# Kernel tuning notes

Measured on AMD Instinct MI355X. Metric: run time of the kernel, lower is better.

## Reference

```python
import jax, jax.numpy as jnp
import numpy as np
import math

DIM = 1024
HEADS = 16
B, N = 2, 2048

POLY = jnp.array([-0.037, 0.481, -2.3, 4.917, -1.791], dtype=jnp.float32)


def adaptive_temperature_softmax(logits):
    # logits: [b, h, n, n]
    original_probs = jax.nn.softmax(logits, axis=-1)
    entropy = jnp.sum(-original_probs * jnp.log(original_probs + 1e-9), axis=-1, keepdims=True)
    e2 = entropy * entropy
    poly_result = POLY[0] * e2 * e2 + POLY[1] * e2 * entropy + POLY[2] * e2 + POLY[3] * entropy + POLY[4]
    beta = jnp.where(entropy > 0.5, jnp.maximum(poly_result, 1.0), 1.0)
    return jax.nn.softmax(logits * beta, axis=-1)


def setup_inputs() -> dict:
    key = jax.random.key(0)
    ks = jax.random.split(key, 5)
    s = 1.0 / math.sqrt(DIM)
    return {
        "x": jax.random.normal(ks[0], (B, N, DIM), dtype=jnp.float32),
        "Wq": jax.random.normal(ks[1], (DIM, DIM), dtype=jnp.float32) * s,
        "Wk": jax.random.normal(ks[2], (DIM, DIM), dtype=jnp.float32) * s,
        "Wv": jax.random.normal(ks[3], (DIM, DIM), dtype=jnp.float32) * s,
        "Wo": jax.random.normal(ks[4], (DIM, DIM), dtype=jnp.float32) * s,
        "bo": jnp.zeros((DIM,), dtype=jnp.float32),
    }


def reference(x, Wq, Wk, Wv, Wo, bo):
    b, n, d = x.shape
    h = HEADS
    hd = d // h
    # torch nn.Linear: y = x @ W.T (+ bias)
    def proj(W):
        t = x @ W.T  # [b, n, d]
        return t.reshape(b, n, h, hd).transpose(0, 2, 1, 3)  # [b, h, n, hd]
    q, k, v = proj(Wq), proj(Wk), proj(Wv)
    sim = jnp.einsum('bhid,bhjd->bhij', q, k) / math.sqrt(hd)
    neg = -jnp.finfo(sim.dtype).max
    causal = jnp.triu(jnp.ones((n, n), dtype=bool), k=1)  # True above diagonal
    sim = jnp.where(causal, neg, sim)
    attn = adaptive_temperature_softmax(sim)
    out = jnp.einsum('bhij,bhjd->bhid', attn, v)
    out = out.transpose(0, 2, 1, 3).reshape(b, n, d)
    return out @ Wo.T + bo
```

## Files before the change

### kernel.cpp

```cpp
#include <hip/hip_runtime.h>
#include <math.h>

#define B_   2
#define N_   2048
#define D_   1024
#define H_   16
#define HD_  64
#define BH_  32
#define M_   4096

typedef __bf16 bf16x8 __attribute__((ext_vector_type(8)));
typedef float  f32x4  __attribute__((ext_vector_type(4)));

__device__ inline unsigned short f2b(float f) {
    unsigned u = __float_as_uint(f);
    u += 0x7FFFu + ((u >> 16) & 1u);
    return (unsigned short)(u >> 16);
}
__device__ inline unsigned short f2b_fast(float f) {
    return (unsigned short)((__float_as_uint(f) + 0x8000u) >> 16);
}

__global__ __launch_bounds__(256)
void cvt_all(const float* __restrict__ x,  const float* __restrict__ wq,
             const float* __restrict__ wk, const float* __restrict__ wv,
             const float* __restrict__ wo, ushort* __restrict__ dst)
{
    int i = blockIdx.x * 256 + threadIdx.x;
    if (i >= 2097152) return;
    int fi = i * 4;
    const float* s; int off;
    if (fi < 4194304) { s = x; off = fi; }
    else {
        int r = fi - 4194304;
        int wsel = r >> 20;
        off = r & 1048575;
        s = (wsel == 0) ? wq : (wsel == 1) ? wk : (wsel == 2) ? wv : wo;
    }
    float4 f = *(const float4*)(s + off);
    ushort4 o;
    o.x = f2b(f.x); o.y = f2b(f.y); o.z = f2b(f.z); o.w = f2b(f.w);
    *(ushort4*)(dst + fi) = o;
}

__global__ __launch_bounds__(256)
void gemm_qkv(const ushort* __restrict__ A,
              const ushort* __restrict__ W0, const ushort* __restrict__ W1,
              const ushort* __restrict__ W2,
              ushort* __restrict__ O0, ushort* __restrict__ O1,
              ushort* __restrict__ O2)
{
    const int z = blockIdx.z;
    const ushort* W = (z == 0) ? W0 : (z == 1) ? W1 : W2;

    __shared__ alignas(16) ushort As[128][40];
    __shared__ alignas(16) ushort Bs[128][40];

    const int t = threadIdx.x;
    const int lane = t & 63, w = t >> 6;
    const int quad = lane >> 4, l15 = lane & 15;
    const int wm = (w >> 1) * 64, wn = (w & 1) * 64;
    const int tileM = blockIdx.x * 128, tileN = blockIdx.y * 128;

    const int r0 = t >> 2, r1 = 64 + (t >> 2);
    const int cg = (t & 3) * 8;
    const ushort* GA0 = A + (size_t)(tileM + r0) * D_ + cg;
    const ushort* GA1 = A + (size_t)(tileM + r1) * D_ + cg;
    const ushort* GB0 = W + (size_t)(tileN + r0) * D_ + cg;
    const ushort* GB1 = W + (size_t)(tileN + r1) * D_ + cg;

    f32x4 acc[4][4];
#pragma unroll
    for (int mt = 0; mt < 4; ++mt)
#pragma unroll
        for (int nt = 0; nt < 4; ++nt) acc[mt][nt] = (f32x4){0.f, 0.f, 0.f, 0.f};

    uint4 pa0 = *(const uint4*)GA0, pa1 = *(const uint4*)GA1;
    uint4 pb0 = *(const uint4*)GB0, pb1 = *(const uint4*)GB1;

    for (int k0 = 0; k0 < D_; k0 += 32) {
        __syncthreads();
        *(uint4*)&As[r0][cg] = pa0;
        *(uint4*)&As[r1][cg] = pa1;
        *(uint4*)&Bs[r0][cg] = pb0;
        *(uint4*)&Bs[r1][cg] = pb1;
        __syncthreads();
        if (k0 + 32 < D_) {
            pa0 = *(const uint4*)(GA0 + k0 + 32);
            pa1 = *(const uint4*)(GA1 + k0 + 32);
            pb0 = *(const uint4*)(GB0 + k0 + 32);
            pb1 = *(const uint4*)(GB1 + k0 + 32);
        }

        bf16x8 af[4], bf[4];
#pragma unroll
        for (int mt = 0; mt < 4; ++mt) af[mt] = *(const bf16x8*)&As[wm + mt * 16 + l15][quad * 8];
#pragma unroll
        for (int nt = 0; nt < 4; ++nt) bf[nt] = *(const bf16x8*)&Bs[wn + nt * 16 + l15][quad * 8];
#pragma unroll
        for (int mt = 0; mt < 4; ++mt)
#pragma unroll
            for (int nt = 0; nt < 4; ++nt)
                acc[mt][nt] = __builtin_amdgcn_mfma_f32_16x16x32_bf16(af[mt], bf[nt], acc[mt][nt], 0, 0, 0);
    }

    ushort* O = (z == 0) ? O0 : (z == 1) ? O1 : O2;
    const float scl = (z == 0) ? 0.18033688f : 1.0f;
#pragma unroll
    for (int mt = 0; mt < 4; ++mt)
#pragma unroll
        for (int nt = 0; nt < 4; ++nt) {
            if (z == 2) {
                int rg0 = tileM + wm + mt * 16 + quad * 4;
                int cgc = tileN + wn + nt * 16 + l15;
                int b = rg0 >> 11, n0 = rg0 & (N_ - 1);
                int h = cgc >> 6, dd = cgc & 63;
                ushort4 o4;
                o4.x = f2b(acc[mt][nt][0]); o4.y = f2b(acc[mt][nt][1]);
                o4.z = f2b(acc[mt][nt][2]); o4.w = f2b(acc[mt][nt][3]);
                *(ushort4*)&O[((size_t)((b * H_ + h) * HD_ + dd)) * N_ + n0] = o4;
            } else {
#pragma unroll
                for (int r = 0; r < 4; ++r) {
                    int rg = tileM + wm + mt * 16 + quad * 4 + r;
                    int cgc = tileN + wn + nt * 16 + l15;
                    int b = rg >> 11, n = rg & (N_ - 1);
                    int h = cgc >> 6, dd = cgc & 63;
                    O[(((size_t)(b * H_ + h)) * N_ + n) * HD_ + dd] = f2b(acc[mt][nt][r] * scl);
                }
            }
        }
}

__global__ __launch_bounds__(256)
void gemm_fin(const ushort* __restrict__ A, const ushort* __restrict__ W,
              const float* __restrict__ bias, float* __restrict__ Of)
{
    __shared__ alignas(16) ushort As[128][40];
    __shared__ alignas(16) ushort Bs[64][40];

    const int t = threadIdx.x;
    const int lane = t & 63, w = t >> 6;
    const int quad = lane >> 4, l15 = lane & 15;
    const int wm = (w >> 1) * 64, wn = (w & 1) * 32;
    const int tileM = blockIdx.x * 128, tileN = blockIdx.y * 64;

    const int r0 = t >> 2, r1 = 64 + (t >> 2);
    const int cg = (t & 3) * 8;
    const ushort* GA0 = A + (size_t)(tileM + r0) * D_ + cg;
    const ushort* GA1 = A + (size_t)(tileM + r1) * D_ + cg;
    const ushort* GB0 = W + (size_t)(tileN + r0) * D_ + cg;

    f32x4 acc[4][2];
#pragma unroll
    for (int mt = 0; mt < 4; ++mt)
#pragma unroll
        for (int nt = 0; nt < 2; ++nt) acc[mt][nt] = (f32x4){0.f, 0.f, 0.f, 0.f};

    uint4 pa0 = *(const uint4*)GA0, pa1 = *(const uint4*)GA1;
    uint4 pb0 = *(const uint4*)GB0;

    for (int k0 = 0; k0 < D_; k0 += 32) {
        __syncthreads();
        *(uint4*)&As[r0][cg] = pa0;
        *(uint4*)&As[r1][cg] = pa1;
        *(uint4*)&Bs[r0 & 63][cg] = pb0;
        __syncthreads();
        if (k0 + 32 < D_) {
            pa0 = *(const uint4*)(GA0 + k0 + 32);
            pa1 = *(const uint4*)(GA1 + k0 + 32);
            pb0 = *(const uint4*)(GB0 + k0 + 32);
        }

        bf16x8 af[4], bf[2];
#pragma unroll
        for (int mt = 0; mt < 4; ++mt) af[mt] = *(const bf16x8*)&As[wm + mt * 16 + l15][quad * 8];
#pragma unroll
        for (int nt = 0; nt < 2; ++nt) bf[nt] = *(const bf16x8*)&Bs[wn + nt * 16 + l15][quad * 8];
#pragma unroll
        for (int mt = 0; mt < 4; ++mt)
#pragma unroll
            for (int nt = 0; nt < 2; ++nt)
                acc[mt][nt] = __builtin_amdgcn_mfma_f32_16x16x32_bf16(af[mt], bf[nt], acc[mt][nt], 0, 0, 0);
    }

#pragma unroll
    for (int mt = 0; mt < 4; ++mt)
#pragma unroll
        for (int nt = 0; nt < 2; ++nt)
#pragma unroll
            for (int r = 0; r < 4; ++r) {
                int rg = tileM + wm + mt * 16 + quad * 4 + r;
                int cgc = tileN + wn + nt * 16 + l15;
                Of[(size_t)rg * D_ + cgc] = acc[mt][nt][r] + bias[cgc];
            }
}

__global__ __launch_bounds__(256)
void attn_mfma(const ushort* __restrict__ Q, const ushort* __restrict__ K,
               const ushort* __restrict__ VT, ushort* __restrict__ AO)
{
    const int bid = blockIdx.x;
    const int p  = bid >> 5;
    const int bh = bid & 31;
    const size_t kvbase = (size_t)bh * N_ * HD_;

    __shared__ alignas(16) ushort Ks[64][72];
    __shared__ alignas(16) ushort Vt[64][72];
    __shared__ alignas(16) ushort Ps[4][4][296];

    const int t = threadIdx.x;
    const int lane = t & 63, w = t >> 6;
    const int quad = lane >> 4, l15 = lane & 15;
    const float SH2 = 11.5416913f;
    const float LN2 = 0.69314718f;

    const int skey = t >> 3;
    const int skc  = (t & 7) * 8;
    const ushort* KS0 = K  + kvbase + (size_t)skey * HD_ + skc;
    const ushort* KS1 = KS0 + 32 * HD_;
    const ushort* VS0 = VT + kvbase + (size_t)skey * N_ + skc;
    const ushort* VS1 = VS0 + 32 * N_;

    const int qrow = w * 16 + quad * 4;
    const int b = bh >> 4, h = bh & 15;

    for (int item = 0; item < 2; ++item) {
        const int qt = item ? p : (31 - p);

        bf16x8 aq0, aq1;
        {
            const size_t qr = kvbase + (size_t)(qt * 64 + w * 16 + l15) * HD_;
            aq0 = *(const bf16x8*)&Q[qr + quad * 8];
            aq1 = *(const bf16x8*)&Q[qr + 32 + quad * 8];
        }

        float ez[4] = {0.f, 0.f, 0.f, 0.f};
        float sz[4] = {0.f, 0.f, 0.f, 0.f};

        uint4 pk0 = *(const uint4*)KS0;
        uint4 pk1 = *(const uint4*)KS1;
        for (int kb = 0; kb <= qt; ++kb) {
            __syncthreads();
            *(uint4*)&Ks[skey][skc]      = pk0;
            *(uint4*)&Ks[32 + skey][skc] = pk1;
            __syncthreads();
            if (kb < qt) {
                pk0 = *(const uint4*)(KS0 + (size_t)(kb + 1) * (64 * HD_));
                pk1 = *(const uint4*)(KS1 + (size_t)(kb + 1) * (64 * HD_));
            }
            if (kb < qt) {
#pragma unroll
                for (int nt = 0; nt < 4; ++nt) {
                    f32x4 sv = (f32x4){0.f, 0.f, 0.f, 0.f};
                    sv = __builtin_amdgcn_mfma_f32_16x16x32_bf16(aq0, *(const bf16x8*)&Ks[nt * 16 + l15][quad * 8], sv, 0, 0, 0);
                    sv = __builtin_amdgcn_mfma_f32_16x16x32_bf16(aq1, *(const bf16x8*)&Ks[nt * 16 + l15][32 + quad * 8], sv, 0, 0, 0);
#pragma unroll
                    for (int r = 0; r < 4; ++r) {
                        float sh = sv[r] - SH2;
                        float e = __builtin_amdgcn_exp2f(sh);
                        ez[r] += e;
                        sz[r] = fmaf(e, sh, sz[r]);
                    }
                }
            } else {
#pragma unroll
                for (int nt = 0; nt < 4; ++nt) {
                    f32x4 sv = (f32x4){0.f, 0.f, 0.f, 0.f};
                    sv = __builtin_amdgcn_mfma_f32_16x16x32_bf16(aq0, *(const bf16x8*)&Ks[nt * 16 + l15][quad * 8], sv, 0, 0, 0);
                    sv = __builtin_amdgcn_mfma_f32_16x16x32_bf16(aq1, *(const bf16x8*)&Ks[nt * 16 + l15][32 + quad * 8], sv, 0, 0, 0);
                    const int kcol = nt * 16 + l15;
#pragma unroll
                    for (int r = 0; r < 4; ++r) {
                        float sh = sv[r] - SH2;
                        float e = (kcol <= qrow + r) ? __builtin_amdgcn_exp2f(sh) : 0.f;
                        ez[r] += e;
                        sz[r] = fmaf(e, sh, sz[r]);
                    }
                }
            }
        }
#pragma unroll
        for (int r = 0; r < 4; ++r) {
#pragma unroll
            for (int off = 1; off < 16; off <<= 1) {
                ez[r] += __shfl_xor(ez[r], off);
                sz[r] += __shfl_xor(sz[r], off);
            }
        }

        float nbs[4], bl[4];
#pragma unroll
        for (int r = 0; r < 4; ++r) {
            float Z = ez[r];
            float Hh = LN2 * (__builtin_amdgcn_logf(Z) - sz[r] / Z);
            float bb = 1.f;
            if (Hh > 0.5f) {
                float e2 = Hh * Hh;
                float pp = -0.037f * e2 * e2 + 0.481f * e2 * Hh - 2.3f * e2 + 4.917f * Hh - 1.791f;
                bb = fmaxf(pp, 1.f);
            }
            bl[r] = bb;
            nbs[r] = -bb * SH2;
        }

        f32x4 ov[4];
#pragma unroll
        for (int nt = 0; nt < 4; ++nt) ov[nt] = (f32x4){0.f, 0.f, 0.f, 0.f};
        float zp[4] = {0.f, 0.f, 0.f, 0.f};

        pk0 = *(const uint4*)KS0;
        pk1 = *(const uint4*)KS1;
        uint4 pv0 = *(const uint4*)VS0;
        uint4 pv1 = *(const uint4*)VS1;
        for (int kb = 0; kb <= qt; ++kb) {
            __syncthreads();
            *(uint4*)&Ks[skey][skc]      = pk0;
            *(uint4*)&Ks[32 + skey][skc] = pk1;
            *(uint4*)&Vt[skey][skc]      = pv0;
            *(uint4*)&Vt[32 + skey][skc] = pv1;
            __syncthreads();
            if (kb < qt) {
                pk0 = *(const uint4*)(KS0 + (size_t)(kb + 1) * (64 * HD_));
                pk1 = *(const uint4*)(KS1 + (size_t)(kb + 1) * (64 * HD_));
                pv0 = *(const uint4*)(VS0 + (kb + 1) * 64);
                pv1 = *(const uint4*)(VS1 + (kb + 1) * 64);
            }
            const bool diag = (kb == qt);

            float wv[4][4];
#pragma unroll
            for (int nt = 0; nt < 4; ++nt) {
                f32x4 sv = (f32x4){0.f, 0.f, 0.f, 0.f};
                sv = __builtin_amdgcn_mfma_f32_16x16x32_bf16(aq0, *(const bf16x8*)&Ks[nt * 16 + l15][quad * 8], sv, 0, 0, 0);
                sv = __builtin_amdgcn_mfma_f32_16x16x32_bf16(aq1, *(const bf16x8*)&Ks[nt * 16 + l15][32 + quad * 8], sv, 0, 0, 0);
                const int kcol = nt * 16 + l15;
#pragma unroll
                for (int r = 0; r < 4; ++r) {
                    float e = __builtin_amdgcn_exp2f(fmaf(bl[r], sv[r], nbs[r]));
                    wv[nt][r] = (!diag || (kcol <= qrow + r)) ? e : 0.f;
                }
            }
#pragma unroll
            for (int nt = 0; nt < 4; ++nt)
#pragma unroll
                for (int r = 0; r < 4; ++r)
                    Ps[w][quad][r * 72 + nt * 16 + l15] = f2b_fast(wv[nt][r]);
#pragma unroll
            for (int r = 0; r < 4; ++r)
                zp[r] += (wv[0][r] + wv[1][r]) + (wv[2][r] + wv[3][r]);

            bf16x8 pa0 = *(const bf16x8*)&Ps[w][l15 >> 2][(l15 & 3) * 72 + quad * 8];
            bf16x8 pa1 = *(const bf16x8*)&Ps[w][l15 >> 2][(l15 & 3) * 72 + 32 + quad * 8];
#pragma unroll
            for (int nt = 0; nt < 4; ++nt) {
                ov[nt] = __builtin_amdgcn_mfma_f32_16x16x32_bf16(pa0, *(const bf16x8*)&Vt[nt * 16 + l15][quad * 8], ov[nt], 0, 0, 0);
                ov[nt] = __builtin_amdgcn_mfma_f32_16x16x32_bf16(pa1, *(const bf16x8*)&Vt[nt * 16 + l15][32 + quad * 8], ov[nt], 0, 0, 0);
            }
        }
#pragma unroll
        for (int r = 0; r < 4; ++r)
#pragma unroll
            for (int off = 1; off < 16; off <<= 1) zp[r] += __shfl_xor(zp[r], off);

#pragma unroll
        for (int r = 0; r < 4; ++r) {
            int qg = qt * 64 + w * 16 + quad * 4 + r;
            float inv = 1.f / zp[r];
            size_t rowoff = ((size_t)(b * N_ + qg)) * D_ + h * HD_;
#pragma unroll
            for (int nt = 0; nt < 4; ++nt)
                AO[rowoff + nt * 16 + l15] = f2b(ov[nt][r] * inv);
        }
    }
}

extern "C" void kernel_launch(void* const* d_in, const int* in_sizes, int n_in,
                              void* d_out, int out_size, void* d_ws, size_t ws_size,
                              hipStream_t stream)
{
    const float* x  = (const float*)d_in[0];
    const float* Wq = (const float*)d_in[1];
    const float* Wk = (const float*)d_in[2];
    const float* Wv = (const float*)d_in[3];
    const float* Wo = (const float*)d_in[4];
    const float* bo = (const float*)d_in[5];
    float* out = (float*)d_out;

    ushort* ws  = (ushort*)d_ws;
    ushort* xb  = ws;
    ushort* wqb = ws + 4194304;
    ushort* wkb = ws + 5242880;
    ushort* wvb = ws + 6291456;
    ushort* wob = ws + 7340032;
    ushort* Qb  = ws + 8388608;
    ushort* Kb  = ws + 12582912;
    ushort* Vtb = ws + 16777216;
    ushort* aob = ws + 20971520;

    cvt_all<<<8192, 256, 0, stream>>>(x, Wq, Wk, Wv, Wo, xb);

    gemm_qkv<<<dim3(32, 8, 3), 256, 0, stream>>>(
        xb, wqb, wkb, wvb, Qb, Kb, Vtb);

    attn_mfma<<<dim3(512), 256, 0, stream>>>(Qb, Kb, Vtb, aob);

    gemm_fin<<<dim3(32, 16), 256, 0, stream>>>(aob, wob, bo, out);
}
```

Measured before the change: 207.1 us.

## Fuse fp32-to-bf16 conversion into GEMMs and split attention into one q-tile per block

Removes the separate conversion kernel, so the QKV and output GEMMs now load fp32 inputs and weights directly and pack them to bf16 before writing to shared memory. The attention kernel drops the paired-item scheme and launches 1024 blocks, each handling a single query tile. Its entropy pass now streams 128-key chunks through a merged K/V shared buffer. This saves a launch and a full fp32-to-bf16 round trip through memory, but doubles global load bytes in the GEMMs and gives up the causal load balancing of pairing.

```diff
diff --git a/kernel.cpp b/kernel.cpp
--- a/kernel.cpp
+++ b/kernel.cpp
@@ -20,38 +20,24 @@
 __device__ inline unsigned short f2b_fast(float f) {
     return (unsigned short)((__float_as_uint(f) + 0x8000u) >> 16);
 }
+__device__ inline uint4 pk8(float4 a, float4 b) {
+    uint4 u;
+    u.x = (uint)f2b(a.x) | ((uint)f2b(a.y) << 16);
+    u.y = (uint)f2b(a.z) | ((uint)f2b(a.w) << 16);
+    u.z = (uint)f2b(b.x) | ((uint)f2b(b.y) << 16);
+    u.w = (uint)f2b(b.z) | ((uint)f2b(b.w) << 16);
+    return u;
+}
 
 __global__ __launch_bounds__(256)
-void cvt_all(const float* __restrict__ x,  const float* __restrict__ wq,
-             const float* __restrict__ wk, const float* __restrict__ wv,
-             const float* __restrict__ wo, ushort* __restrict__ dst)
-{
-    int i = blockIdx.x * 256 + threadIdx.x;
-    if (i >= 2097152) return;
-    int fi = i * 4;
-    const float* s; int off;
-    if (fi < 4194304) { s = x; off = fi; }
-    else {
-        int r = fi - 4194304;
-        int wsel = r >> 20;
-        off = r & 1048575;
-        s = (wsel == 0) ? wq : (wsel == 1) ? wk : (wsel == 2) ? wv : wo;
-    }
-    float4 f = *(const float4*)(s + off);
-    ushort4 o;
-    o.x = f2b(f.x); o.y = f2b(f.y); o.z = f2b(f.z); o.w = f2b(f.w);
-    *(ushort4*)(dst + fi) = o;
-}
-
-__global__ __launch_bounds__(256)
-void gemm_qkv(const ushort* __restrict__ A,
-              const ushort* __restrict__ W0, const ushort* __restrict__ W1,
-              const ushort* __restrict__ W2,
+void gemm_qkv(const float* __restrict__ X,
+              const float* __restrict__ W0, const float* __restrict__ W1,
+              const float* __restrict__ W2,
               ushort* __restrict__ O0, ushort* __restrict__ O1,
               ushort* __restrict__ O2)
 {
     const int z = blockIdx.z;
-    const ushort* W = (z == 0) ? W0 : (z == 1) ? W1 : W2;
+    const float* W = (z == 0) ? W0 : (z == 1) ? W1 : W2;
 
     __shared__ alignas(16) ushort As[128][40];
     __shared__ alignas(16) ushort Bs[128][40];
@@ -64,10 +50,10 @@
 
     const int r0 = t >> 2, r1 = 64 + (t >> 2);
     const int cg = (t & 3) * 8;
-    const ushort* GA0 = A + (size_t)(tileM + r0) * D_ + cg;
-    const ushort* GA1 = A + (size_t)(tileM + r1) * D_ + cg;
-    const ushort* GB0 = W + (size_t)(tileN + r0) * D_ + cg;
-    const ushort* GB1 = W + (size_t)(tileN + r1) * D_ + cg;
+    const float* GA0 = X + (size_t)(tileM + r0) * D_ + cg;
+    const float* GA1 = X + (size_t)(tileM + r1) * D_ + cg;
+    const float* GB0 = W + (size_t)(tileN + r0) * D_ + cg;
+    const float* GB1 = W + (size_t)(tileN + r1) * D_ + cg;
 
     f32x4 acc[4][4];
 #pragma unroll
@@ -75,21 +61,23 @@
 #pragma unroll
         for (int nt = 0; nt < 4; ++nt) acc[mt][nt] = (f32x4){0.f, 0.f, 0.f, 0.f};
 
-    uint4 pa0 = *(const uint4*)GA0, pa1 = *(const uint4*)GA1;
-    uint4 pb0 = *(const uint4*)GB0, pb1 = *(const uint4*)GB1;
+    float4 a00 = *(const float4*)GA0, a01 = *(const float4*)(GA0 + 4);
+    float4 a10 = *(const float4*)GA1, a11 = *(const float4*)(GA1 + 4);
+    float4 b00 = *(const float4*)GB0, b01 = *(const float4*)(GB0 + 4);
+    float4 b10 = *(const float4*)GB1, b11 = *(const float4*)(GB1 + 4);
 
     for (int k0 = 0; k0 < D_; k0 += 32) {
         __syncthreads();
-        *(uint4*)&As[r0][cg] = pa0;
-        *(uint4*)&As[r1][cg] = pa1;
-        *(uint4*)&Bs[r0][cg] = pb0;
-        *(uint4*)&Bs[r1][cg] = pb1;
+        *(uint4*)&As[r0][cg] = pk8(a00, a01);
+        *(uint4*)&As[r1][cg] = pk8(a10, a11);
+        *(uint4*)&Bs[r0][cg] = pk8(b00, b01);
+        *(uint4*)&Bs[r1][cg] = pk8(b10, b11);
         __syncthreads();
         if (k0 + 32 < D_) {
-            pa0 = *(const uint4*)(GA0 + k0 + 32);
-            pa1 = *(const uint4*)(GA1 + k0 + 32);
-            pb0 = *(const uint4*)(GB0 + k0 + 32);
-            pb1 = *(const uint4*)(GB1 + k0 + 32);
+            a00 = *(const float4*)(GA0 + k0 + 32); a01 = *(const float4*)(GA0 + k0 + 36);
+            a10 = *(const float4*)(GA1 + k0 + 32); a11 = *(const float4*)(GA1 + k0 + 36);
+            b00 = *(const float4*)(GB0 + k0 + 32); b01 = *(const float4*)(GB0 + k0 + 36);
+            b10 = *(const float4*)(GB1 + k0 + 32); b11 = *(const float4*)(GB1 + k0 + 36);
         }
 
         bf16x8 af[4], bf[4];
@@ -133,7 +121,7 @@
 }
 
 __global__ __launch_bounds__(256)
-void gemm_fin(const ushort* __restrict__ A, const ushort* __restrict__ W,
+void gemm_fin(const ushort* __restrict__ A, const float* __restrict__ W,
               const float* __restrict__ bias, float* __restrict__ Of)
 {
     __shared__ alignas(16) ushort As[128][40];
@@ -149,7 +137,7 @@
     const int cg = (t & 3) * 8;
     const ushort* GA0 = A + (size_t)(tileM + r0) * D_ + cg;
     const ushort* GA1 = A + (size_t)(tileM + r1) * D_ + cg;
-    const ushort* GB0 = W + (size_t)(tileN + r0) * D_ + cg;
+    const float*  GB0 = W + (size_t)(tileN + r0) * D_ + cg;
 
     f32x4 acc[4][2];
 #pragma unroll
@@ -157,19 +145,20 @@
 #pragma unroll
         for (int nt = 0; nt < 2; ++nt) acc[mt][nt] = (f32x4){0.f, 0.f, 0.f, 0.f};
 
-    uint4 pa0 = *(const uint4*)GA0, pa1 = *(const uint4*)GA1;
-    uint4 pb0 = *(const uint4*)GB0;
+    uint4  pa0 = *(const uint4*)GA0, pa1 = *(const uint4*)GA1;
+    float4 b00 = *(const float4*)GB0, b01 = *(const float4*)(GB0 + 4);
 
     for (int k0 = 0; k0 < D_; k0 += 32) {
         __syncthreads();
         *(uint4*)&As[r0][cg] = pa0;
         *(uint4*)&As[r1][cg] = pa1;
-        *(uint4*)&Bs[r0 & 63][cg] = pb0;
+        *(uint4*)&Bs[r0 & 63][cg] = pk8(b00, b01);
         __syncthreads();
         if (k0 + 32 < D_) {
             pa0 = *(const uint4*)(GA0 + k0 + 32);
             pa1 = *(const uint4*)(GA1 + k0 + 32);
-            pb0 = *(const uint4*)(GB0 + k0 + 32);
+            b00 = *(const float4*)(GB0 + k0 + 32);
+            b01 = *(const float4*)(GB0 + k0 + 36);
         }
 
         bf16x8 af[4], bf[2];
@@ -201,12 +190,11 @@
                const ushort* __restrict__ VT, ushort* __restrict__ AO)
 {
     const int bid = blockIdx.x;
-    const int p  = bid >> 5;
+    const int qt = 31 - (bid >> 5);
     const int bh = bid & 31;
     const size_t kvbase = (size_t)bh * N_ * HD_;
 
-    __shared__ alignas(16) ushort Ks[64][72];
-    __shared__ alignas(16) ushort Vt[64][72];
+    __shared__ alignas(16) ushort KV[128][72];
     __shared__ alignas(16) ushort Ps[4][4][296];
 
     const int t = threadIdx.x;
@@ -217,161 +205,169 @@
 
     const int skey = t >> 3;
     const int skc  = (t & 7) * 8;
-    const ushort* KS0 = K  + kvbase + (size_t)skey * HD_ + skc;
-    const ushort* KS1 = KS0 + 32 * HD_;
+    const ushort* KS = K  + kvbase + (size_t)skey * HD_ + skc;
     const ushort* VS0 = VT + kvbase + (size_t)skey * N_ + skc;
     const ushort* VS1 = VS0 + 32 * N_;
 
     const int qrow = w * 16 + quad * 4;
     const int b = bh >> 4, h = bh & 15;
 
-    for (int item = 0; item < 2; ++item) {
-        const int qt = item ? p : (31 - p);
-
-        bf16x8 aq0, aq1;
-        {
-            const size_t qr = kvbase + (size_t)(qt * 64 + w * 16 + l15) * HD_;
-            aq0 = *(const bf16x8*)&Q[qr + quad * 8];
-            aq1 = *(const bf16x8*)&Q[qr + 32 + quad * 8];
-        }
-
-        float ez[4] = {0.f, 0.f, 0.f, 0.f};
-        float sz[4] = {0.f, 0.f, 0.f, 0.f};
-
-        uint4 pk0 = *(const uint4*)KS0;
-        uint4 pk1 = *(const uint4*)KS1;
-        for (int kb = 0; kb <= qt; ++kb) {
-            __syncthreads();
-            *(uint4*)&Ks[skey][skc]      = pk0;
-            *(uint4*)&Ks[32 + skey][skc] = pk1;
-            __syncthreads();
-            if (kb < qt) {
-                pk0 = *(const uint4*)(KS0 + (size_t)(kb + 1) * (64 * HD_));
-                pk1 = *(const uint4*)(KS1 + (size_t)(kb + 1) * (64 * HD_));
-            }
-            if (kb < qt) {
-#pragma unroll
-                for (int nt = 0; nt < 4; ++nt) {
-                    f32x4 sv = (f32x4){0.f, 0.f, 0.f, 0.f};
-                    sv = __builtin_amdgcn_mfma_f32_16x16x32_bf16(aq0, *(const bf16x8*)&Ks[nt * 16 + l15][quad * 8], sv, 0, 0, 0);
-                    sv = __builtin_amdgcn_mfma_f32_16x16x32_bf16(aq1, *(const bf16x8*)&Ks[nt * 16 + l15][32 + quad * 8], sv, 0, 0, 0);
-#pragma unroll
-                    for (int r = 0; r < 4; ++r) {
-                        float sh = sv[r] - SH2;
-                        float e = __builtin_amdgcn_exp2f(sh);
-                        ez[r] += e;
-                        sz[r] = fmaf(e, sh, sz[r]);
-                    }
+    bf16x8 aq0, aq1;
+    {
+        const size_t qr = kvbase + (size_t)(qt * 64 + w * 16 + l15) * HD_;
+        aq0 = *(const bf16x8*)&Q[qr + quad * 8];
+        aq1 = *(const bf16x8*)&Q[qr + 32 + quad * 8];
+    }
+
+    float ez[4] = {0.f, 0.f, 0.f, 0.f};
+    float sz[4] = {0.f, 0.f, 0.f, 0.f};
+
+    const int nfull = qt >> 1;
+    const int lastTiles = (((qt + 1) * 64) - nfull * 128) >> 4;
+
+    uint4 q0 = *(const uint4*)KS;
+    uint4 q1 = *(const uint4*)(KS + 32 * HD_);
+    uint4 q2 = *(const uint4*)(KS + 64 * HD_);
+    uint4 q3 = *(const uint4*)(KS + 96 * HD_);
+
+    for (int c = 0; c <= nfull; ++c) {
+        __syncthreads();
+        *(uint4*)&KV[skey][skc]      = q0;
+        *(uint4*)&KV[32 + skey][skc] = q1;
+        *(uint4*)&KV[64 + skey][skc] = q2;
+        *(uint4*)&KV[96 + skey][skc] = q3;
+        __syncthreads();
+        if (c < nfull) {
+            const ushort* nb = KS + (size_t)(c + 1) * (128 * HD_);
+            q0 = *(const uint4*)nb;
+            q1 = *(const uint4*)(nb + 32 * HD_);
+            q2 = *(const uint4*)(nb + 64 * HD_);
+            q3 = *(const uint4*)(nb + 96 * HD_);
+        }
+        if (c < nfull) {
+#pragma unroll
+            for (int nt = 0; nt < 8; ++nt) {
+                f32x4 sv = (f32x4){0.f, 0.f, 0.f, 0.f};
+                sv = __builtin_amdgcn_mfma_f32_16x16x32_bf16(aq0, *(const bf16x8*)&KV[nt * 16 + l15][quad * 8], sv, 0, 0, 0);
+                sv = __builtin_amdgcn_mfma_f32_16x16x32_bf16(aq1, *(const bf16x8*)&KV[nt * 16 + l15][32 + quad * 8], sv, 0, 0, 0);
+#pragma unroll
+                for (int r = 0; r < 4; ++r) {
+                    float sh = sv[r] - SH2;
+                    float e = __builtin_amdgcn_exp2f(sh);
+                    ez[r] += e;
+                    sz[r] = fmaf(e, sh, sz[r]);
                 }
-            } else {
-#pragma unroll
-                for (int nt = 0; nt < 4; ++nt) {
-                    f32x4 sv = (f32x4){0.f, 0.f, 0.f, 0.f};
-                    sv = __builtin_amdgcn_mfma_f32_16x16x32_bf16(aq0, *(const bf16x8*)&Ks[nt * 16 + l15][quad * 8], sv, 0, 0, 0);
-                    sv = __builtin_amdgcn_mfma_f32_16x16x32_bf16(aq1, *(const bf16x8*)&Ks[nt * 16 + l15][32 + quad * 8], sv, 0, 0, 0);
-                    const int kcol = nt * 16 + l15;
-#pragma unroll
-                    for (int r = 0; r < 4; ++r) {
-                        float sh = sv[r] - SH2;
-                        float e = (kcol <= qrow + r) ? __builtin_amdgcn_exp2f(sh) : 0.f;
-                        ez[r] += e;
-                        sz[r] = fmaf(e, sh, sz[r]);
-                    }
+            }
+        } else {
+            const int kbase = c * 128;
+            const int qglob = qt * 64 + qrow;
+            for (int nt = 0; nt < lastTiles; ++nt) {
+                f32x4 sv = (f32x4){0.f, 0.f, 0.f, 0.f};
+                sv = __builtin_amdgcn_mfma_f32_16x16x32_bf16(aq0, *(const bf16x8*)&KV[nt * 16 + l15][quad * 8], sv, 0, 0, 0);
+                sv = __builtin_amdgcn_mfma_f32_16x16x32_bf16(aq1, *(const bf16x8*)&KV[nt * 16 + l15][32 + quad * 8], sv, 0, 0, 0);
+                const int kcol = kbase + nt * 16 + l15;
+#pragma unroll
+                for (int r = 0; r < 4; ++r) {
+                    float sh = sv[r] - SH2;
+                    float e = (kcol <= qglob + r) ? __builtin_amdgcn_exp2f(sh) : 0.f;
+                    ez[r] += e;
+                    sz[r] = fmaf(e, sh, sz[r]);
                 }
             }
         }
-#pragma unroll
-        for (int r = 0; r < 4; ++r) {
-#pragma unroll
-            for (int off = 1; off < 16; off <<= 1) {
-                ez[r] += __shfl_xor(ez[r], off);
-                sz[r] += __shfl_xor(sz[r], off);
-            }
-        }
-
-        float nbs[4], bl[4];
-#pragma unroll
-        for (int r = 0; r < 4; ++r) {
-            float Z = ez[r];
-            float Hh = LN2 * (__builtin_amdgcn_logf(Z) - sz[r] / Z);
-            float bb = 1.f;
-            if (Hh > 0.5f) {
-                float e2 = Hh * Hh;
-                float pp = -0.037f * e2 * e2 + 0.481f * e2 * Hh - 2.3f * e2 + 4.917f * Hh - 1.791f;
-                bb = fmaxf(pp, 1.f);
-            }
-            bl[r] = bb;
-            nbs[r] = -bb * SH2;
-        }
-
-        f32x4 ov[4];
-#pragma unroll
-        for (int nt = 0; nt < 4; ++nt) ov[nt] = (f32x4){0.f, 0.f, 0.f, 0.f};
-        float zp[4] = {0.f, 0.f, 0.f, 0.f};
-
-        pk0 = *(const uint4*)KS0;
-        pk1 = *(const uint4*)KS1;
-        uint4 pv0 = *(const uint4*)VS0;
-        uint4 pv1 = *(const uint4*)VS1;
-        for (int kb = 0; kb <= qt; ++kb) {
-            __syncthreads();
-            *(uint4*)&Ks[skey][skc]      = pk0;
-            *(uint4*)&Ks[32 + skey][skc] = pk1;
-            *(uint4*)&Vt[skey][skc]      = pv0;
-            *(uint4*)&Vt[32 + skey][skc] = pv1;
-            __syncthreads();
-            if (kb < qt) {
-                pk0 = *(const uint4*)(KS0 + (size_t)(kb + 1) * (64 * HD_));
-                pk1 = *(const uint4*)(KS1 + (size_t)(kb + 1) * (64 * HD_));
-                pv0 = *(const uint4*)(VS0 + (kb + 1) * 64);
-                pv1 = *(const uint4*)(VS1 + (kb + 1) * 64);
-            }
-            const bool diag = (kb == qt);
-
-            float wv[4][4];
-#pragma unroll
-            for (int nt = 0; nt < 4; ++nt) {
-                f32x4 sv = (f32x4){0.f, 0.f, 0.f, 0.f};
-                sv = __builtin_amdgcn_mfma_f32_16x16x32_bf16(aq0, *(const bf16x8*)&Ks[nt * 16 + l15][quad * 8], sv, 0, 0, 0);
-                sv = __builtin_amdgcn_mfma_f32_16x16x32_bf16(aq1, *(const bf16x8*)&Ks[nt * 16 + l15][32 + quad * 8], sv, 0, 0, 0);
-                const int kcol = nt * 16 + l15;
-#pragma unroll
-                for (int r = 0; r < 4; ++r) {
-                    float e = __builtin_amdgcn_exp2f(fmaf(bl[r], sv[r], nbs[r]));
-                    wv[nt][r] = (!diag || (kcol <= qrow + r)) ? e : 0.f;
-                }
-            }
-#pragma unroll
-            for (int nt = 0; nt < 4; ++nt)
-#pragma unroll
-                for (int r = 0; r < 4; ++r)
-                    Ps[w][quad][r * 72 + nt * 16 + l15] = f2b_fast(wv[nt][r]);
+    }
+#pragma unroll
+    for (int r = 0; r < 4; ++r) {
+#pragma unroll
+        for (int off = 1; off < 16; off <<= 1) {
+            ez[r] += __shfl_xor(ez[r], off);
+            sz[r] += __shfl_xor(sz[r], off);
+        }
+    }
+
+    float nbs[4], bl[4];
+#pragma unroll
+    for (int r = 0; r < 4; ++r) {
+        float Z = ez[r];
+        float Hh = LN2 * (__builtin_amdgcn_logf(Z) - sz[r] / Z);
+        float bb = 1.f;
+        if (Hh > 0.5f) {
+            float e2 = Hh * Hh;
+            float pp = -0.037f * e2 * e2 + 0.481f * e2 * Hh - 2.3f * e2 + 4.917f * Hh - 1.791f;
+            bb = fmaxf(pp, 1.f);
+        }
+        bl[r] = bb;
+        nbs[r] = -bb * SH2;
+    }
+
+    f32x4 ov[4];
+#pragma unroll
+    for (int nt = 0; nt < 4; ++nt) ov[nt] = (f32x4){0.f, 0.f, 0.f, 0.f};
+    float zp[4] = {0.f, 0.f, 0.f, 0.f};
+
+    uint4 pk0 = *(const uint4*)KS;
+    uint4 pk1 = *(const uint4*)(KS + 32 * HD_);
+    uint4 pv0 = *(const uint4*)VS0;
+    uint4 pv1 = *(const uint4*)VS1;
+    for (int kb = 0; kb <= qt; ++kb) {
+        __syncthreads();
+        *(uint4*)&KV[skey][skc]      = pk0;
+        *(uint4*)&KV[32 + skey][skc] = pk1;
+        *(uint4*)&KV[64 + skey][skc] = pv0;
+        *(uint4*)&KV[96 + skey][skc] = pv1;
+        __syncthreads();
+        if (kb < qt) {
+            const ushort* nk = KS + (size_t)(kb + 1) * (64 * HD_);
+            pk0 = *(const uint4*)nk;
+            pk1 = *(const uint4*)(nk + 32 * HD_);
+            pv0 = *(const uint4*)(VS0 + (kb + 1) * 64);
+            pv1 = *(const uint4*)(VS1 + (kb + 1) * 64);
+        }
+        const bool diag = (kb == qt);
+
+        float wv[4][4];
+#pragma unroll
+        for (int nt = 0; nt < 4; ++nt) {
+            f32x4 sv = (f32x4){0.f, 0.f, 0.f, 0.f};
+            sv = __builtin_amdgcn_mfma_f32_16x16x32_bf16(aq0, *(const bf16x8*)&KV[nt * 16 + l15][quad * 8], sv, 0, 0, 0);
+            sv = __builtin_amdgcn_mfma_f32_16x16x32_bf16(aq1, *(const bf16x8*)&KV[nt * 16 + l15][32 + quad * 8], sv, 0, 0, 0);
+            const int kcol = nt * 16 + l15;
+#pragma unroll
+            for (int r = 0; r < 4; ++r) {
+                float e = __builtin_amdgcn_exp2f(fmaf(bl[r], sv[r], nbs[r]));
+                wv[nt][r] = (!diag || (kcol <= qrow + r)) ? e : 0.f;
+            }
+        }
+#pragma unroll
+        for (int nt = 0; nt < 4; ++nt)
 #pragma unroll
             for (int r = 0; r < 4; ++r)
-                zp[r] += (wv[0][r] + wv[1][r]) + (wv[2][r] + wv[3][r]);
-
-            bf16x8 pa0 = *(const bf16x8*)&Ps[w][l15 >> 2][(l15 & 3) * 72 + quad * 8];
-            bf16x8 pa1 = *(const bf16x8*)&Ps[w][l15 >> 2][(l15 & 3) * 72 + 32 + quad * 8];
-#pragma unroll
-            for (int nt = 0; nt < 4; ++nt) {
-                ov[nt] = __builtin_amdgcn_mfma_f32_16x16x32_bf16(pa0, *(const bf16x8*)&Vt[nt * 16 + l15][quad * 8], ov[nt], 0, 0, 0);
-                ov[nt] = __builtin_amdgcn_mfma_f32_16x16x32_bf16(pa1, *(const bf16x8*)&Vt[nt * 16 + l15][32 + quad * 8], ov[nt], 0, 0, 0);
-            }
-        }
+                Ps[w][quad][r * 72 + nt * 16 + l15] = f2b_fast(wv[nt][r]);
 #pragma unroll
         for (int r = 0; r < 4; ++r)
-#pragma unroll
-            for (int off = 1; off < 16; off <<= 1) zp[r] += __shfl_xor(zp[r], off);
-
-#pragma unroll
-        for (int r = 0; r < 4; ++r) {
-            int qg = qt * 64 + w * 16 + quad * 4 + r;
-            float inv = 1.f / zp[r];
-            size_t rowoff = ((size_t)(b * N_ + qg)) * D_ + h * HD_;
-#pragma unroll
-            for (int nt = 0; nt < 4; ++nt)
-                AO[rowoff + nt * 16 + l15] = f2b(ov[nt][r] * inv);
-        }
+            zp[r] += (wv[0][r] + wv[1][r]) + (wv[2][r] + wv[3][r]);
+
+        bf16x8 pa0 = *(const bf16x8*)&Ps[w][l15 >> 2][(l15 & 3) * 72 + quad * 8];
+        bf16x8 pa1 = *(const bf16x8*)&Ps[w][l15 >> 2][(l15 & 3) * 72 + 32 + quad * 8];
+#pragma unroll
+        for (int nt = 0; nt < 4; ++nt) {
+            ov[nt] = __builtin_amdgcn_mfma_f32_16x16x32_bf16(pa0, *(const bf16x8*)&KV[64 + nt * 16 + l15][quad * 8], ov[nt], 0, 0, 0);
+            ov[nt] = __builtin_amdgcn_mfma_f32_16x16x32_bf16(pa1, *(const bf16x8*)&KV[64 + nt * 16 + l15][32 + quad * 8], ov[nt], 0, 0, 0);
+        }
+    }
+#pragma unroll
+    for (int r = 0; r < 4; ++r)
+#pragma unroll
+        for (int off = 1; off < 16; off <<= 1) zp[r] += __shfl_xor(zp[r], off);
+
+#pragma unroll
+    for (int r = 0; r < 4; ++r) {
+        int qg = qt * 64 + w * 16 + quad * 4 + r;
+        float inv = 1.f / zp[r];
+        size_t rowoff = ((size_t)(b * N_ + qg)) * D_ + h * HD_;
+#pragma unroll
+        for (int nt = 0; nt < 4; ++nt)
+            AO[rowoff + nt * 16 + l15] = f2b(ov[nt][r] * inv);
     }
 }
 
@@ -388,22 +384,15 @@
     float* out = (float*)d_out;
 
     ushort* ws  = (ushort*)d_ws;
-    ushort* xb  = ws;
-    ushort* wqb = ws + 4194304;
-    ushort* wkb = ws + 5242880;
-    ushort* wvb = ws + 6291456;
-    ushort* wob = ws + 7340032;
-    ushort* Qb  = ws + 8388608;
-    ushort* Kb  = ws + 12582912;
-    ushort* Vtb = ws + 16777216;
-    ushort* aob = ws + 20971520;
-
-    cvt_all<<<8192, 256, 0, stream>>>(x, Wq, Wk, Wv, Wo, xb);
+    ushort* Qb  = ws;
+    ushort* Kb  = ws + 4194304;
+    ushort* Vtb = ws + 8388608;
+    ushort* aob = ws + 12582912;
 
     gemm_qkv<<<dim3(32, 8, 3), 256, 0, stream>>>(
-        xb, wqb, wkb, wvb, Qb, Kb, Vtb);
-
-    attn_mfma<<<dim3(512), 256, 0, stream>>>(Qb, Kb, Vtb, aob);
-
-    gemm_fin<<<dim3(32, 16), 256, 0, stream>>>(aob, wob, bo, out);
-}
+        x, Wq, Wk, Wv, Qb, Kb, Vtb);
+
+    attn_mfma<<<dim3(1024), 256, 0, stream>>>(Qb, Kb, Vtb, aob);
+
+    gemm_fin<<<dim3(32, 16), 256, 0, stream>>>(aob, Wo, bo, out);
+}
```

New measurement: 215.4 us. 1.04x slower.

## Split attention into one q-tile per block and fuse Wo conversion into final GEMM

Applied to the files above, without the earlier changes.

The attention kernel now launches one block per (query tile, head) in descending tile-size order, replacing the paired-tile blocks that balanced the causal workload by hand. The output-projection GEMM reads fp32 Wo directly and converts it to bf16 while staging into shared memory, so the conversion kernel no longer processes Wo. This increases the block count and occupancy options for attention, but depends on hardware scheduling for balance. The GEMM now reads twice the weight bytes and repeats the conversion in every M-tile block.

```diff
diff --git a/kernel.cpp b/kernel.cpp
--- a/kernel.cpp
+++ b/kernel.cpp
@@ -20,14 +20,22 @@
 __device__ inline unsigned short f2b_fast(float f) {
     return (unsigned short)((__float_as_uint(f) + 0x8000u) >> 16);
 }
+__device__ inline uint4 pk8(float4 a, float4 b) {
+    uint4 u;
+    u.x = (uint)f2b(a.x) | ((uint)f2b(a.y) << 16);
+    u.y = (uint)f2b(a.z) | ((uint)f2b(a.w) << 16);
+    u.z = (uint)f2b(b.x) | ((uint)f2b(b.y) << 16);
+    u.w = (uint)f2b(b.z) | ((uint)f2b(b.w) << 16);
+    return u;
+}
 
 __global__ __launch_bounds__(256)
-void cvt_all(const float* __restrict__ x,  const float* __restrict__ wq,
-             const float* __restrict__ wk, const float* __restrict__ wv,
-             const float* __restrict__ wo, ushort* __restrict__ dst)
+void cvt_xw(const float* __restrict__ x,  const float* __restrict__ wq,
+            const float* __restrict__ wk, const float* __restrict__ wv,
+            ushort* __restrict__ dst)
 {
     int i = blockIdx.x * 256 + threadIdx.x;
-    if (i >= 2097152) return;
+    if (i >= 1835008) return;
     int fi = i * 4;
     const float* s; int off;
     if (fi < 4194304) { s = x; off = fi; }
@@ -35,7 +43,7 @@
         int r = fi - 4194304;
         int wsel = r >> 20;
         off = r & 1048575;
-        s = (wsel == 0) ? wq : (wsel == 1) ? wk : (wsel == 2) ? wv : wo;
+        s = (wsel == 0) ? wq : (wsel == 1) ? wk : wv;
     }
     float4 f = *(const float4*)(s + off);
     ushort4 o;
@@ -133,7 +141,7 @@
 }
 
 __global__ __launch_bounds__(256)
-void gemm_fin(const ushort* __restrict__ A, const ushort* __restrict__ W,
+void gemm_fin(const ushort* __restrict__ A, const float* __restrict__ W,
               const float* __restrict__ bias, float* __restrict__ Of)
 {
     __shared__ alignas(16) ushort As[128][40];
@@ -149,7 +157,7 @@
     const int cg = (t & 3) * 8;
     const ushort* GA0 = A + (size_t)(tileM + r0) * D_ + cg;
     const ushort* GA1 = A + (size_t)(tileM + r1) * D_ + cg;
-    const ushort* GB0 = W + (size_t)(tileN + r0) * D_ + cg;
+    const float*  GB0 = W + (size_t)(tileN + r0) * D_ + cg;
 
     f32x4 acc[4][2];
 #pragma unroll
@@ -157,19 +165,20 @@
 #pragma unroll
         for (int nt = 0; nt < 2; ++nt) acc[mt][nt] = (f32x4){0.f, 0.f, 0.f, 0.f};
 
-    uint4 pa0 = *(const uint4*)GA0, pa1 = *(const uint4*)GA1;
-    uint4 pb0 = *(const uint4*)GB0;
+    uint4  pa0 = *(const uint4*)GA0, pa1 = *(const uint4*)GA1;
+    float4 b00 = *(const float4*)GB0, b01 = *(const float4*)(GB0 + 4);
 
     for (int k0 = 0; k0 < D_; k0 += 32) {
         __syncthreads();
         *(uint4*)&As[r0][cg] = pa0;
         *(uint4*)&As[r1][cg] = pa1;
-        *(uint4*)&Bs[r0 & 63][cg] = pb0;
+        *(uint4*)&Bs[r0 & 63][cg] = pk8(b00, b01);
         __syncthreads();
         if (k0 + 32 < D_) {
             pa0 = *(const uint4*)(GA0 + k0 + 32);
             pa1 = *(const uint4*)(GA1 + k0 + 32);
-            pb0 = *(const uint4*)(GB0 + k0 + 32);
+            b00 = *(const float4*)(GB0 + k0 + 32);
+            b01 = *(const float4*)(GB0 + k0 + 36);
         }
 
         bf16x8 af[4], bf[2];
@@ -201,7 +210,7 @@
                const ushort* __restrict__ VT, ushort* __restrict__ AO)
 {
     const int bid = blockIdx.x;
-    const int p  = bid >> 5;
+    const int qt = 31 - (bid >> 5);
     const int bh = bid & 31;
     const size_t kvbase = (size_t)bh * N_ * HD_;
 
@@ -225,110 +234,42 @@
     const int qrow = w * 16 + quad * 4;
     const int b = bh >> 4, h = bh & 15;
 
-    for (int item = 0; item < 2; ++item) {
-        const int qt = item ? p : (31 - p);
-
-        bf16x8 aq0, aq1;
-        {
-            const size_t qr = kvbase + (size_t)(qt * 64 + w * 16 + l15) * HD_;
-            aq0 = *(const bf16x8*)&Q[qr + quad * 8];
-            aq1 = *(const bf16x8*)&Q[qr + 32 + quad * 8];
-        }
-
-        float ez[4] = {0.f, 0.f, 0.f, 0.f};
-        float sz[4] = {0.f, 0.f, 0.f, 0.f};
-
-        uint4 pk0 = *(const uint4*)KS0;
-        uint4 pk1 = *(const uint4*)KS1;
-        for (int kb = 0; kb <= qt; ++kb) {
-            __syncthreads();
-            *(uint4*)&Ks[skey][skc]      = pk0;
-            *(uint4*)&Ks[32 + skey][skc] = pk1;
-            __syncthreads();
-            if (kb < qt) {
-                pk0 = *(const uint4*)(KS0 + (size_t)(kb + 1) * (64 * HD_));
-                pk1 = *(const uint4*)(KS1 + (size_t)(kb + 1) * (64 * HD_));
-            }
-            if (kb < qt) {
-#pragma unroll
-                for (int nt = 0; nt < 4; ++nt) {
-                    f32x4 sv = (f32x4){0.f, 0.f, 0.f, 0.f};
-                    sv = __builtin_amdgcn_mfma_f32_16x16x32_bf16(aq0, *(const bf16x8*)&Ks[nt * 16 + l15][quad * 8], sv, 0, 0, 0);
-                    sv = __builtin_amdgcn_mfma_f32_16x16x32_bf16(aq1, *(const bf16x8*)&Ks[nt * 16 + l15][32 + quad * 8], sv, 0, 0, 0);
-#pragma unroll
-                    for (int r = 0; r < 4; ++r) {
-                        float sh = sv[r] - SH2;
-                        float e = __builtin_amdgcn_exp2f(sh);
-                        ez[r] += e;
-                        sz[r] = fmaf(e, sh, sz[r]);
-                    }
-                }
-            } else {
-#pragma unroll
-                for (int nt = 0; nt < 4; ++nt) {
-                    f32x4 sv = (f32x4){0.f, 0.f, 0.f, 0.f};
-                    sv = __builtin_amdgcn_mfma_f32_16x16x32_bf16(aq0, *(const bf16x8*)&Ks[nt * 16 + l15][quad * 8], sv, 0, 0, 0);
-                    sv = __builtin_amdgcn_mfma_f32_16x16x32_bf16(aq1, *(const bf16x8*)&Ks[nt * 16 + l15][32 + quad * 8], sv, 0, 0, 0);
-                    const int kcol = nt * 16 + l15;
-#pragma unroll
-                    for (int r = 0; r < 4; ++r) {
-                        float sh = sv[r] - SH2;
-                        float e = (kcol <= qrow + r) ? __builtin_amdgcn_exp2f(sh) : 0.f;
-                        ez[r] += e;
-                        sz[r] = fmaf(e, sh, sz[r]);
-                    }
+    bf16x8 aq0, aq1;
+    {
+        const size_t qr = kvbase + (size_t)(qt * 64 + w * 16 + l15) * HD_;
+        aq0 = *(const bf16x8*)&Q[qr + quad * 8];
+        aq1 = *(const bf16x8*)&Q[qr + 32 + quad * 8];
+    }
+
+    float ez[4] = {0.f, 0.f, 0.f, 0.f};
+    float sz[4] = {0.f, 0.f, 0.f, 0.f};
+
+    uint4 pk0 = *(const uint4*)KS0;
+    uint4 pk1 = *(const uint4*)KS1;
+    for (int kb = 0; kb <= qt; ++kb) {
+        __syncthreads();
+        *(uint4*)&Ks[skey][skc]      = pk0;
+        *(uint4*)&Ks[32 + skey][skc] = pk1;
+        __syncthreads();
+        if (kb < qt) {
+            pk0 = *(const uint4*)(KS0 + (size_t)(kb + 1) * (64 * HD_));
+            pk1 = *(const uint4*)(KS1 + (size_t)(kb + 1) * (64 * HD_));
+        }
+        if (kb < qt) {
+#pragma unroll
+            for (int nt = 0; nt < 4; ++nt) {
+                f32x4 sv = (f32x4){0.f, 0.f, 0.f, 0.f};
+                sv = __builtin_amdgcn_mfma_f32_16x16x32_bf16(aq0, *(const bf16x8*)&Ks[nt * 16 + l15][quad * 8], sv, 0, 0, 0);
+                sv = __builtin_amdgcn_mfma_f32_16x16x32_bf16(aq1, *(const bf16x8*)&Ks[nt * 16 + l15][32 + quad * 8], sv, 0, 0, 0);
+#pragma unroll
+                for (int r = 0; r < 4; ++r) {
+                    float sh = sv[r] - SH2;
+                    float e = __builtin_amdgcn_exp2f(sh);
+                    ez[r] += e;
+                    sz[r] = fmaf(e, sh, sz[r]);
                 }
             }
-        }
-#pragma unroll
-        for (int r = 0; r < 4; ++r) {
-#pragma unroll
-            for (int off = 1; off < 16; off <<= 1) {
-                ez[r] += __shfl_xor(ez[r], off);
-                sz[r] += __shfl_xor(sz[r], off);
-            }
-        }
-
-        float nbs[4], bl[4];
-#pragma unroll
-        for (int r = 0; r < 4; ++r) {
-            float Z = ez[r];
-            float Hh = LN2 * (__builtin_amdgcn_logf(Z) - sz[r] / Z);
-            float bb = 1.f;
-            if (Hh > 0.5f) {
-                float e2 = Hh * Hh;
-                float pp = -0.037f * e2 * e2 + 0.481f * e2 * Hh - 2.3f * e2 + 4.917f * Hh - 1.791f;
-                bb = fmaxf(pp, 1.f);
-            }
-            bl[r] = bb;
-            nbs[r] = -bb * SH2;
-        }
-
-        f32x4 ov[4];
-#pragma unroll
-        for (int nt = 0; nt < 4; ++nt) ov[nt] = (f32x4){0.f, 0.f, 0.f, 0.f};
-        float zp[4] = {0.f, 0.f, 0.f, 0.f};
-
-        pk0 = *(const uint4*)KS0;
-        pk1 = *(const uint4*)KS1;
-        uint4 pv0 = *(const uint4*)VS0;
-        uint4 pv1 = *(const uint4*)VS1;
-        for (int kb = 0; kb <= qt; ++kb) {
-            __syncthreads();
-            *(uint4*)&Ks[skey][skc]      = pk0;
-            *(uint4*)&Ks[32 + skey][skc] = pk1;
-            *(uint4*)&Vt[skey][skc]      = pv0;
-            *(uint4*)&Vt[32 + skey][skc] = pv1;
-            __syncthreads();
-            if (kb < qt) {
-                pk0 = *(const uint4*)(KS0 + (size_t)(kb + 1) * (64 * HD_));
-                pk1 = *(const uint4*)(KS1 + (size_t)(kb + 1) * (64 * HD_));
-                pv0 = *(const uint4*)(VS0 + (kb + 1) * 64);
-                pv1 = *(const uint4*)(VS1 + (kb + 1) * 64);
-            }
-            const bool diag = (kb == qt);
-
-            float wv[4][4];
+        } else {
 #pragma unroll
             for (int nt = 0; nt < 4; ++nt) {
                 f32x4 sv = (f32x4){0.f, 0.f, 0.f, 0.f};
@@ -337,41 +278,105 @@
                 const int kcol = nt * 16 + l15;
 #pragma unroll
                 for (int r = 0; r < 4; ++r) {
-                    float e = __builtin_amdgcn_exp2f(fmaf(bl[r], sv[r], nbs[r]));
-                    wv[nt][r] = (!diag || (kcol <= qrow + r)) ? e : 0.f;
+                    float sh = sv[r] - SH2;
+                    float e = (kcol <= qrow + r) ? __builtin_amdgcn_exp2f(sh) : 0.f;
+                    ez[r] += e;
+                    sz[r] = fmaf(e, sh, sz[r]);
                 }
             }
-#pragma unroll
-            for (int nt = 0; nt < 4; ++nt)
-#pragma unroll
-                for (int r = 0; r < 4; ++r)
-                    Ps[w][quad][r * 72 + nt * 16 + l15] = f2b_fast(wv[nt][r]);
+        }
+    }
+#pragma unroll
+    for (int r = 0; r < 4; ++r) {
+#pragma unroll
+        for (int off = 1; off < 16; off <<= 1) {
+            ez[r] += __shfl_xor(ez[r], off);
+            sz[r] += __shfl_xor(sz[r], off);
+        }
+    }
+
+    float nbs[4], bl[4];
+#pragma unroll
+    for (int r = 0; r < 4; ++r) {
+        float Z = ez[r];
+        float Hh = LN2 * (__builtin_amdgcn_logf(Z) - sz[r] / Z);
+        float bb = 1.f;
+        if (Hh > 0.5f) {
+            float e2 = Hh * Hh;
+            float pp = -0.037f * e2 * e2 + 0.481f * e2 * Hh - 2.3f * e2 + 4.917f * Hh - 1.791f;
+            bb = fmaxf(pp, 1.f);
+        }
+        bl[r] = bb;
+        nbs[r] = -bb * SH2;
+    }
+
+    f32x4 ov[4];
+#pragma unroll
+    for (int nt = 0; nt < 4; ++nt) ov[nt] = (f32x4){0.f, 0.f, 0.f, 0.f};
+    float zp[4] = {0.f, 0.f, 0.f, 0.f};
+
+    pk0 = *(const uint4*)KS0;
+    pk1 = *(const uint4*)KS1;
+    uint4 pv0 = *(const uint4*)VS0;
+    uint4 pv1 = *(const uint4*)VS1;
+    for (int kb = 0; kb <= qt; ++kb) {
+        __syncthreads();
+        *(uint4*)&Ks[skey][skc]      = pk0;
+        *(uint4*)&Ks[32 + skey][skc] = pk1;
+        *(uint4*)&Vt[skey][skc]      = pv0;
+        *(uint4*)&Vt[32 + skey][skc] = pv1;
+        __syncthreads();
+        if (kb < qt) {
+            pk0 = *(const uint4*)(KS0 + (size_t)(kb + 1) * (64 * HD_));
+            pk1 = *(const uint4*)(KS1 + (size_t)(kb + 1) * (64 * HD_));
+            pv0 = *(const uint4*)(VS0 + (kb + 1) * 64);
+            pv1 = *(const uint4*)(VS1 + (kb + 1) * 64);
+        }
+        const bool diag = (kb == qt);
+
+        float wv[4][4];
+#pragma unroll
+        for (int nt = 0; nt < 4; ++nt) {
+            f32x4 sv = (f32x4){0.f, 0.f, 0.f, 0.f};
+            sv = __builtin_amdgcn_mfma_f32_16x16x32_bf16(aq0, *(const bf16x8*)&Ks[nt * 16 + l15][quad * 8], sv, 0, 0, 0);
+            sv = __builtin_amdgcn_mfma_f32_16x16x32_bf16(aq1, *(const bf16x8*)&Ks[nt * 16 + l15][32 + quad * 8], sv, 0, 0, 0);
+            const int kcol = nt * 16 + l15;
+#pragma unroll
+            for (int r = 0; r < 4; ++r) {
+                float e = __builtin_amdgcn_exp2f(fmaf(bl[r], sv[r], nbs[r]));
+                wv[nt][r] = (!diag || (kcol <= qrow + r)) ? e : 0.f;
+            }
+        }
+#pragma unroll
+        for (int nt = 0; nt < 4; ++nt)
 #pragma unroll
             for (int r = 0; r < 4; ++r)
-                zp[r] += (wv[0][r] + wv[1][r]) + (wv[2][r] + wv[3][r]);
-
-            bf16x8 pa0 = *(const bf16x8*)&Ps[w][l15 >> 2][(l15 & 3) * 72 + quad * 8];
-            bf16x8 pa1 = *(const bf16x8*)&Ps[w][l15 >> 2][(l15 & 3) * 72 + 32 + quad * 8];
-#pragma unroll
-            for (int nt = 0; nt < 4; ++nt) {
-                ov[nt] = __builtin_amdgcn_mfma_f32_16x16x32_bf16(pa0, *(const bf16x8*)&Vt[nt * 16 + l15][quad * 8], ov[nt], 0, 0, 0);
-                ov[nt] = __builtin_amdgcn_mfma_f32_16x16x32_bf16(pa1, *(const bf16x8*)&Vt[nt * 16 + l15][32 + quad * 8], ov[nt], 0, 0, 0);
-            }
-        }
+                Ps[w][quad][r * 72 + nt * 16 + l15] = f2b_fast(wv[nt][r]);
 #pragma unroll
         for (int r = 0; r < 4; ++r)
-#pragma unroll
-            for (int off = 1; off < 16; off <<= 1) zp[r] += __shfl_xor(zp[r], off);
-
-#pragma unroll
-        for (int r = 0; r < 4; ++r) {
-            int qg = qt * 64 + w * 16 + quad * 4 + r;
-            float inv = 1.f / zp[r];
-            size_t rowoff = ((size_t)(b * N_ + qg)) * D_ + h * HD_;
-#pragma unroll
-            for (int nt = 0; nt < 4; ++nt)
-                AO[rowoff + nt * 16 + l15] = f2b(ov[nt][r] * inv);
-        }
+            zp[r] += (wv[0][r] + wv[1][r]) + (wv[2][r] + wv[3][r]);
+
+        bf16x8 pa0 = *(const bf16x8*)&Ps[w][l15 >> 2][(l15 & 3) * 72 + quad * 8];
+        bf16x8 pa1 = *(const bf16x8*)&Ps[w][l15 >> 2][(l15 & 3) * 72 + 32 + quad * 8];
+#pragma unroll
+        for (int nt = 0; nt < 4; ++nt) {
+            ov[nt] = __builtin_amdgcn_mfma_f32_16x16x32_bf16(pa0, *(const bf16x8*)&Vt[nt * 16 + l15][quad * 8], ov[nt], 0, 0, 0);
+            ov[nt] = __builtin_amdgcn_mfma_f32_16x16x32_bf16(pa1, *(const bf16x8*)&Vt[nt * 16 + l15][32 + quad * 8], ov[nt], 0, 0, 0);
+        }
+    }
+#pragma unroll
+    for (int r = 0; r < 4; ++r)
+#pragma unroll
+        for (int off = 1; off < 16; off <<= 1) zp[r] += __shfl_xor(zp[r], off);
+
+#pragma unroll
+    for (int r = 0; r < 4; ++r) {
+        int qg = qt * 64 + w * 16 + quad * 4 + r;
+        float inv = 1.f / zp[r];
+        size_t rowoff = ((size_t)(b * N_ + qg)) * D_ + h * HD_;
+#pragma unroll
+        for (int nt = 0; nt < 4; ++nt)
+            AO[rowoff + nt * 16 + l15] = f2b(ov[nt][r] * inv);
     }
 }
 
@@ -392,18 +397,17 @@
     ushort* wqb = ws + 4194304;
     ushort* wkb = ws + 5242880;
     ushort* wvb = ws + 6291456;
-    ushort* wob = ws + 7340032;
-    ushort* Qb  = ws + 8388608;
-    ushort* Kb  = ws + 12582912;
-    ushort* Vtb = ws + 16777216;
-    ushort* aob = ws + 20971520;
-
-    cvt_all<<<8192, 256, 0, stream>>>(x, Wq, Wk, Wv, Wo, xb);
+    ushort* Qb  = ws + 7340032;
+    ushort* Kb  = ws + 11534336;
+    ushort* Vtb = ws + 15728640;
+    ushort* aob = ws + 19922944;
+
+    cvt_xw<<<7168, 256, 0, stream>>>(x, Wq, Wk, Wv, xb);
 
     gemm_qkv<<<dim3(32, 8, 3), 256, 0, stream>>>(
         xb, wqb, wkb, wvb, Qb, Kb, Vtb);
 
-    attn_mfma<<<dim3(512), 256, 0, stream>>>(Qb, Kb, Vtb, aob);
-
-    gemm_fin<<<dim3(32, 16), 256, 0, stream>>>(aob, wob, bo, out);
-}
+    attn_mfma<<<dim3(1024), 256, 0, stream>>>(Qb, Kb, Vtb, aob);
+
+    gemm_fin<<<dim3(32, 16), 256, 0, stream>>>(aob, Wo, bo, out);
+}
```

Result: no change. 210.1 us (+1.5%).
